# Optimization experiments

Measured on AMD Instinct MI355X. Metric: run time of the kernel, lower is better.

## Reference

```python
import jax, jax.numpy as jnp
import numpy as np

B, V, F, H = 8, 5023, 9976, 512  # batch, n_verts, n_faces, image size (K=1 face per pixel)


def _vertex_normals(verts, faces):
    # verts [V,3], faces [F,3] int. Faithful to DECA util.vertex_normals:
    # cross products scatter-added per face corner, then F.normalize(eps=1e-6).
    v0 = verts[faces[:, 0]]
    v1 = verts[faces[:, 1]]
    v2 = verts[faces[:, 2]]
    n = jnp.zeros_like(verts)
    n = n.at[faces[:, 1]].add(jnp.cross(v2 - v1, v0 - v1))
    n = n.at[faces[:, 2]].add(jnp.cross(v0 - v2, v1 - v2))
    n = n.at[faces[:, 0]].add(jnp.cross(v1 - v0, v2 - v0))
    norm = jnp.maximum(jnp.linalg.norm(n, axis=-1, keepdims=True), 1e-6)
    return n / norm


def _face_vertices(attr, faces):
    # attr [B,V,3] -> [B,F,3,3] gather of per-face corner attributes
    return jax.vmap(lambda a: a[faces])(attr)


def _rasterize_attributes(pix_to_face, bary, attributes):
    # attributes [B,F,3,D]; pix_to_face [N,H,W,K] packed face ids (-1 = miss);
    # bary [N,H,W,K,3]. Mirrors Pytorch3dRasterizer.forward post-raster math.
    Bn, Fn, _, D = attributes.shape
    attrs = attributes.reshape(Bn * Fn, 3, D)
    miss = pix_to_face < 0                              # [N,H,W,K]
    p2f = jnp.where(miss, 0, pix_to_face)
    pixel_face_vals = attrs[p2f]                        # [N,H,W,K,3,D] gather
    pixel_vals = jnp.sum(bary[..., None] * pixel_face_vals, axis=-2)  # [N,H,W,K,D]
    pixel_vals = jnp.where(miss[..., None], 0.0, pixel_vals)
    pixel_vals = jnp.moveaxis(pixel_vals[:, :, :, 0], -1, 1)          # [N,D,H,W]
    vismask = (pix_to_face[..., 0] > -1).astype(pixel_vals.dtype)[:, None]
    return jnp.concatenate([pixel_vals, vismask], axis=1)             # [N,D+1,H,W]


def setup_inputs() -> dict:
    keys = jax.random.split(jax.random.key(0), 8)
    vertices = jax.random.normal(keys[0], (B, V, 3), jnp.float32)
    transformed_vertices = jax.random.normal(keys[1], (B, V, 3), jnp.float32)
    albedos = jax.random.uniform(keys[2], (B, 3, 256, 256), jnp.float32)
    face_uvcoords = jax.random.uniform(keys[3], (F, 3, 3), jnp.float32) * 2.0 - 1.0
    bary = jax.random.uniform(keys[4], (B, H, H, 1, 3), jnp.float32) + 1e-3
    bary_coords = bary / bary.sum(-1, keepdims=True)
    faces = jax.random.randint(keys[5], (F, 3), 0, V, jnp.int32)
    p2f = jax.random.randint(keys[6], (B, H, H, 1), 0, B * F, jnp.int32)
    miss = jax.random.uniform(keys[7], (B, H, H, 1)) < 0.3
    pix_to_face = jnp.where(miss, jnp.int32(-1), p2f)
    return {"vertices": vertices, "transformed_vertices": transformed_vertices,
            "albedos": albedos, "face_uvcoords": face_uvcoords,
            "bary_coords": bary_coords, "faces": faces, "pix_to_face": pix_to_face}


def reference(vertices, transformed_vertices, albedos, face_uvcoords, bary_coords, faces, pix_to_face):
    # albedos is unused in this forward path (shading branch disabled in source).
    del albedos
    batch = vertices.shape[0]
    tv = transformed_vertices.at[:, :, 2].add(10.0)
    face_verts = _face_vertices(vertices, faces)                         # [B,F,3,3]
    normals = jax.vmap(_vertex_normals, in_axes=(0, None))(vertices, faces)
    face_normals = _face_vertices(normals, faces)                        # [B,F,3,3]
    t_normals = jax.vmap(_vertex_normals, in_axes=(0, None))(tv, faces)
    t_face_normals = _face_vertices(t_normals, faces)                    # [B,F,3,3]
    norm_uv = face_uvcoords * 0.5 + 0.5                                  # [F,3,3]
    attributes = jnp.concatenate([
        jnp.broadcast_to(norm_uv[None], (batch,) + norm_uv.shape),
        jax.lax.stop_gradient(t_face_normals),
        jax.lax.stop_gradient(face_verts),
        face_normals,
    ], axis=-1)                                                          # [B,F,3,12]
    rendering = _rasterize_attributes(pix_to_face, bary_coords, attributes)  # [B,13,H,W]
    uvcoords_images = rendering[:, :3]
    grid = jnp.transpose(uvcoords_images, (0, 2, 3, 1))[..., :2]
    t_normal_map = jax.lax.stop_gradient(rendering[:, 3:6])
    pos_mask = (t_normal_map[:, 2:] < -0.05).astype(rendering.dtype)
    normal_images = rendering[:, 9:12]
    return (uvcoords_images, pos_mask, grid, normals, normal_images, t_normals)
```

## Files before the change

### kernel.cpp

```cpp
#include <hip/hip_runtime.h>
#include <hip/hip_fp16.h>

#define BB_ 8
#define VV_ 5023
#define FF_ 9976
#define HH_ 512

static constexpr long long OUT_UV   = 0;
static constexpr long long OUT_POS  = OUT_UV   + (long long)BB_*3*HH_*HH_;
static constexpr long long OUT_GRID = OUT_POS  + (long long)BB_*HH_*HH_;
static constexpr long long OUT_N    = OUT_GRID + (long long)BB_*HH_*HH_*2;
static constexpr long long OUT_NIMG = OUT_N    + (long long)BB_*VV_*3;
static constexpr long long OUT_TN   = OUT_NIMG + (long long)BB_*3*HH_*HH_;

__device__ inline float pack_h2(float a, float b) {
    union { float f; __half2 h; } u;
    u.h = __halves2half2(__float2half_rn(a), __float2half_rn(b));
    return u.f;
}
__device__ inline float2 unpack_h2(float w) {
    union { float f; __half2 h; } u; u.f = w;
    return __half22float2(u.h);
}

__global__ __launch_bounds__(256) void facenorm_k(const float* __restrict__ verts,
                                                  const float* __restrict__ tverts,
                                                  const int*   __restrict__ faces,
                                                  float* __restrict__ fnorm,
                                                  int*   __restrict__ counts) {
    int t = blockIdx.x * blockDim.x + threadIdx.x;
    if (t >= BB_ * 2 * FF_) return;
    int bm = t / FF_;
    int f  = t - bm * FF_;
    int m  = bm & 1;
    int b  = bm >> 1;

    const float* vb = (m ? tverts : verts) + (long long)b * VV_ * 3;
    const float zoff = m ? 10.0f : 0.0f;

    int i0 = faces[f*3+0], i1 = faces[f*3+1], i2 = faces[f*3+2];
    float v0x = vb[i0*3+0], v0y = vb[i0*3+1], v0z = vb[i0*3+2] + zoff;
    float v1x = vb[i1*3+0], v1y = vb[i1*3+1], v1z = vb[i1*3+2] + zoff;
    float v2x = vb[i2*3+0], v2y = vb[i2*3+1], v2z = vb[i2*3+2] + zoff;
    float ax = v1x - v0x, ay = v1y - v0y, az = v1z - v0z;
    float bx = v2x - v0x, by = v2y - v0y, bz = v2z - v0z;
    fnorm[(long long)t*3+0] = ay * bz - az * by;
    fnorm[(long long)t*3+1] = az * bx - ax * bz;
    fnorm[(long long)t*3+2] = ax * by - ay * bx;

    if (bm == 0) {
        atomicAdd(&counts[i0], 1);
        atomicAdd(&counts[i1], 1);
        atomicAdd(&counts[i2], 1);
    }
}

__global__ __launch_bounds__(256) void scan_k(const int* __restrict__ counts,
                                              int* __restrict__ offsets,
                                              int* __restrict__ cursor) {
    __shared__ int sums[256];
    const int SEG = (VV_ + 255) / 256;
    int tid = threadIdx.x;

    int local[SEG];
    int s = 0;
    #pragma unroll
    for (int j = 0; j < SEG; ++j) {
        int v = tid * SEG + j;
        int c = (v < VV_) ? counts[v] : 0;
        local[j] = s;
        s += c;
    }
    sums[tid] = s;
    __syncthreads();
    for (int st = 1; st < 256; st <<= 1) {
        int add = (tid >= st) ? sums[tid - st] : 0;
        __syncthreads();
        sums[tid] += add;
        __syncthreads();
    }
    int base = (tid == 0) ? 0 : sums[tid - 1];
    #pragma unroll
    for (int j = 0; j < SEG; ++j) {
        int v = tid * SEG + j;
        if (v < VV_) {
            int o = base + local[j];
            offsets[v] = o;
            cursor[v]  = o;
        }
    }
    if (tid == 0) offsets[VV_] = FF_ * 3;
}

__global__ __launch_bounds__(256) void fill_k(const int* __restrict__ faces,
                                              int* __restrict__ cursor,
                                              int* __restrict__ list) {
    int i = blockIdx.x * blockDim.x + threadIdx.x;
    if (i >= FF_ * 3) return;
    int v = faces[i];
    int slot = atomicAdd(&cursor[v], 1);
    list[slot] = i / 3;
}

__global__ __launch_bounds__(256) void gather_k(const int* __restrict__ offsets,
                                                const int* __restrict__ list,
                                                const float* __restrict__ fnorm,
                                                float* __restrict__ outN,
                                                float* __restrict__ outTN) {
    int t = blockIdx.x * blockDim.x + threadIdx.x;
    if (t >= BB_ * 2 * VV_) return;
    int bm = t / VV_;
    int v  = t - bm * VV_;
    int o0 = offsets[v], o1 = offsets[v + 1];
    const float* fb = fnorm + (long long)bm * FF_ * 3;
    float x = 0.f, y = 0.f, z = 0.f;
    for (int j = o0; j < o1; ++j) {
        int f = list[j];
        x += fb[f*3+0];
        y += fb[f*3+1];
        z += fb[f*3+2];
    }
    float inv = 1.0f / fmaxf(sqrtf(x*x + y*y + z*z), 1e-6f);
    float* o = ((bm & 1) ? outTN : outN) + ((long long)(bm >> 1) * VV_ + v) * 3;
    o[0] = x * inv; o[1] = y * inv; o[2] = z * inv;
}

__global__ void build_recs(const int*   __restrict__ faces,
                           const float* __restrict__ uvc,
                           const float* __restrict__ outN,
                           const float* __restrict__ outTN,
                           float4* __restrict__ uvrec,
                           float4* __restrict__ nrec) {
    int t = blockIdx.x * blockDim.x + threadIdx.x;
    if (t >= BB_ * FF_) return;
    int b = t / FF_;
    int f = t - b * FF_;
    int ia = faces[f*3+0], ib = faces[f*3+1], ic = faces[f*3+2];

    const float* nb = outN  + (long long)b * VV_ * 3;
    const float* tb = outTN + (long long)b * VV_ * 3;
    float nax = nb[ia*3+0], nay = nb[ia*3+1], naz = nb[ia*3+2];
    float nbx = nb[ib*3+0], nby = nb[ib*3+1], nbz = nb[ib*3+2];
    float ncx = nb[ic*3+0], ncy = nb[ic*3+1], ncz = nb[ic*3+2];
    float ta = tb[ia*3+2], tbv = tb[ib*3+2], tc = tb[ic*3+2];

    nrec[(long long)t*2+0] = make_float4(ta, tbv, tc, pack_h2(ncz, 0.f));
    nrec[(long long)t*2+1] = make_float4(pack_h2(nax, nay), pack_h2(naz, nbx),
                                         pack_h2(nby, nbz), pack_h2(ncx, ncy));

    if (b == 0) {
        const float* u = uvc + (long long)f * 9;
        float r0 = u[0]*0.5f+0.5f, r1 = u[1]*0.5f+0.5f, r2 = u[2]*0.5f+0.5f;
        float r3 = u[3]*0.5f+0.5f, r4 = u[4]*0.5f+0.5f, r5 = u[5]*0.5f+0.5f;
        float r6 = u[6]*0.5f+0.5f, r7 = u[7]*0.5f+0.5f, r8 = u[8]*0.5f+0.5f;
        uvrec[(long long)f*2+0] = make_float4(pack_h2(r0,r1), pack_h2(r2,r3),
                                              pack_h2(r4,r5), pack_h2(r6,r7));
        uvrec[(long long)f*2+1] = make_float4(pack_h2(r8,0.f), 0.f, 0.f, 0.f);
    }
}

__device__ inline void shade(int pf, float w0, float w1, float w2,
                             const float4* __restrict__ uvrec,
                             const float4* __restrict__ nrec,
                             float& uv0, float& uv1, float& uv2,
                             float& n0, float& n1, float& n2, float& pm) {
    int pfs = pf < 0 ? 0 : pf;
    int bb = pfs / FF_;
    int ff = pfs - bb * FF_;

    float4 U0 = uvrec[(long long)ff*2+0];
    float  U8 = ((const float*)uvrec)[(long long)ff*8+4];
    float4 A  = nrec[(long long)pfs*2+0];
    float4 Bq = nrec[(long long)pfs*2+1];

    float2 u01 = unpack_h2(U0.x), u23 = unpack_h2(U0.y);
    float2 u45 = unpack_h2(U0.z), u67 = unpack_h2(U0.w);
    float2 u8p = unpack_h2(U8);
    float2 m01 = unpack_h2(Bq.x), m23 = unpack_h2(Bq.y);
    float2 m45 = unpack_h2(Bq.z), m67 = unpack_h2(Bq.w);
    float2 m8p = unpack_h2(A.w);

    uv0 = w0*u01.x + w1*u23.y + w2*u67.x;
    uv1 = w0*u01.y + w1*u45.x + w2*u67.y;
    uv2 = w0*u23.x + w1*u45.y + w2*u8p.x;
    n0  = w0*m01.x + w1*m23.y + w2*m67.x;
    n1  = w0*m01.y + w1*m45.x + w2*m67.y;
    n2  = w0*m23.x + w1*m45.y + w2*m8p.x;
    float tnz = w0*A.x + w1*A.y + w2*A.z;
    pm = (tnz < -0.05f) ? 1.0f : 0.0f;

    if (pf < 0) { uv0 = uv1 = uv2 = n0 = n1 = n2 = pm = 0.0f; }
}

__global__ __launch_bounds__(256) void raster4(const int4*   __restrict__ p2f4,
                                               const float4* __restrict__ bary4,
                                               const float4* __restrict__ uvrec,
                                               const float4* __restrict__ nrec,
                                               float* __restrict__ out) {
    int t = blockIdx.x * blockDim.x + threadIdx.x;
    const int NQ = BB_ * HH_ * HH_ / 4;
    if (t >= NQ) return;
    int pix0 = t << 2;
    int b    = pix0 >> 18;
    int yx0  = pix0 & (HH_*HH_ - 1);

    int4   pf = p2f4[t];
    float4 B0 = bary4[(long long)t*3+0];
    float4 B1 = bary4[(long long)t*3+1];
    float4 B2 = bary4[(long long)t*3+2];

    float uv0a, uv1a, uv2a, n0a, n1a, n2a, pma;
    float uv0b, uv1b, uv2b, n0b, n1b, n2b, pmb;
    float uv0c, uv1c, uv2c, n0c, n1c, n2c, pmc;
    float uv0d, uv1d, uv2d, n0d, n1d, n2d, pmd;

    shade(pf.x, B0.x, B0.y, B0.z, uvrec, nrec, uv0a, uv1a, uv2a, n0a, n1a, n2a, pma);
    shade(pf.y, B0.w, B1.x, B1.y, uvrec, nrec, uv0b, uv1b, uv2b, n0b, n1b, n2b, pmb);
    shade(pf.z, B1.z, B1.w, B2.x, uvrec, nrec, uv0c, uv1c, uv2c, n0c, n1c, n2c, pmc);
    shade(pf.w, B2.y, B2.z, B2.w, uvrec, nrec, uv0d, uv1d, uv2d, n0d, n1d, n2d, pmd);

    const long long HW = (long long)HH_ * HH_;
    *(float4*)(out + OUT_UV  + ((long long)(b*3+0))*HW + yx0) = make_float4(uv0a, uv0b, uv0c, uv0d);
    *(float4*)(out + OUT_UV  + ((long long)(b*3+1))*HW + yx0) = make_float4(uv1a, uv1b, uv1c, uv1d);
    *(float4*)(out + OUT_UV  + ((long long)(b*3+2))*HW + yx0) = make_float4(uv2a, uv2b, uv2c, uv2d);
    *(float4*)(out + OUT_POS + (long long)b*HW + yx0)         = make_float4(pma, pmb, pmc, pmd);
    float* gbase = out + OUT_GRID + ((long long)b*HW + yx0)*2;
    *(float4*)(gbase + 0) = make_float4(uv0a, uv1a, uv0b, uv1b);
    *(float4*)(gbase + 4) = make_float4(uv0c, uv1c, uv0d, uv1d);
    *(float4*)(out + OUT_NIMG + ((long long)(b*3+0))*HW + yx0) = make_float4(n0a, n0b, n0c, n0d);
    *(float4*)(out + OUT_NIMG + ((long long)(b*3+1))*HW + yx0) = make_float4(n1a, n1b, n1c, n1d);
    *(float4*)(out + OUT_NIMG + ((long long)(b*3+2))*HW + yx0) = make_float4(n2a, n2b, n2c, n2d);
}

extern "C" void kernel_launch(void* const* d_in, const int* in_sizes, int n_in,
                              void* d_out, int out_size, void* d_ws, size_t ws_size,
                              hipStream_t stream) {
    const float* vertices  = (const float*)d_in[0];
    const float* tvertices = (const float*)d_in[1];
    const float* face_uvc  = (const float*)d_in[3];
    const float* bary      = (const float*)d_in[4];
    const int*   faces     = (const int*)d_in[5];
    const int*   p2f       = (const int*)d_in[6];

    float* out = (float*)d_out;

    float4* uvrec   = (float4*)d_ws;
    float4* nrec    = uvrec + (size_t)FF_*2;
    float*  fnorm   = (float*)(nrec + (size_t)BB_*FF_*2);
    int*    counts  = (int*)(fnorm + (size_t)BB_*2*FF_*3);
    int*    offsets = counts + VV_;
    int*    cursor  = offsets + VV_ + 1;
    int*    list    = cursor + VV_;

    hipMemsetAsync(counts, 0, (size_t)VV_ * sizeof(int), stream);

    {
        int n = BB_ * 2 * FF_;
        facenorm_k<<<(n + 255) / 256, 256, 0, stream>>>(vertices, tvertices, faces, fnorm, counts);
    }
    scan_k<<<1, 256, 0, stream>>>(counts, offsets, cursor);
    {
        int n = FF_ * 3;
        fill_k<<<(n + 255) / 256, 256, 0, stream>>>(faces, cursor, list);
    }
    {
        int n = BB_ * 2 * VV_;
        gather_k<<<(n + 255) / 256, 256, 0, stream>>>(offsets, list, fnorm, out + OUT_N, out + OUT_TN);
    }
    {
        int n = BB_ * FF_;
        build_recs<<<(n + 255) / 256, 256, 0, stream>>>(faces, face_uvc, out + OUT_N, out + OUT_TN, uvrec, nrec);
    }
    {
        int nq = BB_ * HH_ * HH_ / 4;
        raster4<<<(nq + 255) / 256, 256, 0, stream>>>((const int4*)p2f, (const float4*)bary,
                                                      uvrec, nrec, out);
    }
}
```

Before: 75.20 us.

## Fuse mesh topology build into one block and recompute face normals in gather

Replaces the memset, count, scan and fill kernels with one single-block kernel that builds the vertex-to-face adjacency in shared memory. The separate face-normal kernel and its scratch buffer are removed; each vertex now recomputes the cross products of its incident faces while gathering. Per-face UV and normal data are packed into one 64-byte record per batch-face, so each pixel does three float4 loads from one record, and miss pixels skip the loads. This removes launches and intermediate traffic at the cost of redundant cross-product work, a serial single-block topology pass, and a larger per-batch record table.

```diff
diff --git a/kernel.cpp b/kernel.cpp
--- a/kernel.cpp
+++ b/kernel.cpp
@@ -23,115 +23,99 @@
     return __half22float2(u.h);
 }
 
-__global__ __launch_bounds__(256) void facenorm_k(const float* __restrict__ verts,
-                                                  const float* __restrict__ tverts,
-                                                  const int*   __restrict__ faces,
-                                                  float* __restrict__ fnorm,
-                                                  int*   __restrict__ counts) {
-    int t = blockIdx.x * blockDim.x + threadIdx.x;
-    if (t >= BB_ * 2 * FF_) return;
-    int bm = t / FF_;
-    int f  = t - bm * FF_;
-    int m  = bm & 1;
-    int b  = bm >> 1;
-
-    const float* vb = (m ? tverts : verts) + (long long)b * VV_ * 3;
-    const float zoff = m ? 10.0f : 0.0f;
-
-    int i0 = faces[f*3+0], i1 = faces[f*3+1], i2 = faces[f*3+2];
-    float v0x = vb[i0*3+0], v0y = vb[i0*3+1], v0z = vb[i0*3+2] + zoff;
-    float v1x = vb[i1*3+0], v1y = vb[i1*3+1], v1z = vb[i1*3+2] + zoff;
-    float v2x = vb[i2*3+0], v2y = vb[i2*3+1], v2z = vb[i2*3+2] + zoff;
-    float ax = v1x - v0x, ay = v1y - v0y, az = v1z - v0z;
-    float bx = v2x - v0x, by = v2y - v0y, bz = v2z - v0z;
-    fnorm[(long long)t*3+0] = ay * bz - az * by;
-    fnorm[(long long)t*3+1] = az * bx - ax * bz;
-    fnorm[(long long)t*3+2] = ax * by - ay * bx;
-
-    if (bm == 0) {
-        atomicAdd(&counts[i0], 1);
-        atomicAdd(&counts[i1], 1);
-        atomicAdd(&counts[i2], 1);
-    }
-}
-
-__global__ __launch_bounds__(256) void scan_k(const int* __restrict__ counts,
-                                              int* __restrict__ offsets,
-                                              int* __restrict__ cursor) {
-    __shared__ int sums[256];
-    const int SEG = (VV_ + 255) / 256;
+__global__ __launch_bounds__(1024) void topo_k(const int* __restrict__ faces,
+                                               int* __restrict__ offsets,
+                                               int* __restrict__ list) {
+    __shared__ int cnt[VV_];
+    __shared__ int sums[1024];
     int tid = threadIdx.x;
 
+    for (int v = tid; v < VV_; v += 1024) cnt[v] = 0;
+    __syncthreads();
+    for (int i = tid; i < FF_ * 3; i += 1024) atomicAdd(&cnt[faces[i]], 1);
+    __syncthreads();
+
+    const int SEG = (VV_ + 1023) / 1024;
     int local[SEG];
     int s = 0;
     #pragma unroll
     for (int j = 0; j < SEG; ++j) {
         int v = tid * SEG + j;
-        int c = (v < VV_) ? counts[v] : 0;
+        int c = (v < VV_) ? cnt[v] : 0;
         local[j] = s;
         s += c;
     }
     sums[tid] = s;
     __syncthreads();
-    for (int st = 1; st < 256; st <<= 1) {
+    for (int st = 1; st < 1024; st <<= 1) {
         int add = (tid >= st) ? sums[tid - st] : 0;
         __syncthreads();
         sums[tid] += add;
         __syncthreads();
     }
     int base = (tid == 0) ? 0 : sums[tid - 1];
+    __syncthreads();
     #pragma unroll
     for (int j = 0; j < SEG; ++j) {
         int v = tid * SEG + j;
         if (v < VV_) {
             int o = base + local[j];
             offsets[v] = o;
-            cursor[v]  = o;
+            cnt[v] = o;
         }
     }
     if (tid == 0) offsets[VV_] = FF_ * 3;
-}
-
-__global__ __launch_bounds__(256) void fill_k(const int* __restrict__ faces,
-                                              int* __restrict__ cursor,
-                                              int* __restrict__ list) {
-    int i = blockIdx.x * blockDim.x + threadIdx.x;
-    if (i >= FF_ * 3) return;
-    int v = faces[i];
-    int slot = atomicAdd(&cursor[v], 1);
-    list[slot] = i / 3;
-}
-
-__global__ __launch_bounds__(256) void gather_k(const int* __restrict__ offsets,
-                                                const int* __restrict__ list,
-                                                const float* __restrict__ fnorm,
+    __syncthreads();
+
+    for (int i = tid; i < FF_ * 3; i += 1024) {
+        int v = faces[i];
+        int slot = atomicAdd(&cnt[v], 1);
+        list[slot] = i / 3;
+    }
+}
+
+__global__ __launch_bounds__(64) void vgather_k(const float* __restrict__ verts,
+                                                const float* __restrict__ tverts,
+                                                const int*   __restrict__ faces,
+                                                const int*   __restrict__ offsets,
+                                                const int*   __restrict__ list,
                                                 float* __restrict__ outN,
                                                 float* __restrict__ outTN) {
-    int t = blockIdx.x * blockDim.x + threadIdx.x;
+    int t = blockIdx.x * 64 + threadIdx.x;
     if (t >= BB_ * 2 * VV_) return;
     int bm = t / VV_;
     int v  = t - bm * VV_;
+    int m  = bm & 1;
+    int b  = bm >> 1;
+
+    const float* vb = (m ? tverts : verts) + (long long)b * VV_ * 3;
+    const float zoff = m ? 10.0f : 0.0f;
+
     int o0 = offsets[v], o1 = offsets[v + 1];
-    const float* fb = fnorm + (long long)bm * FF_ * 3;
     float x = 0.f, y = 0.f, z = 0.f;
     for (int j = o0; j < o1; ++j) {
         int f = list[j];
-        x += fb[f*3+0];
-        y += fb[f*3+1];
-        z += fb[f*3+2];
+        int i0 = faces[f*3+0], i1 = faces[f*3+1], i2 = faces[f*3+2];
+        float v0x = vb[i0*3+0], v0y = vb[i0*3+1], v0z = vb[i0*3+2] + zoff;
+        float v1x = vb[i1*3+0], v1y = vb[i1*3+1], v1z = vb[i1*3+2] + zoff;
+        float v2x = vb[i2*3+0], v2y = vb[i2*3+1], v2z = vb[i2*3+2] + zoff;
+        float ax = v1x - v0x, ay = v1y - v0y, az = v1z - v0z;
+        float bx = v2x - v0x, by = v2y - v0y, bz = v2z - v0z;
+        x += ay * bz - az * by;
+        y += az * bx - ax * bz;
+        z += ax * by - ay * bx;
     }
     float inv = 1.0f / fmaxf(sqrtf(x*x + y*y + z*z), 1e-6f);
-    float* o = ((bm & 1) ? outTN : outN) + ((long long)(bm >> 1) * VV_ + v) * 3;
+    float* o = (m ? outTN : outN) + ((long long)b * VV_ + v) * 3;
     o[0] = x * inv; o[1] = y * inv; o[2] = z * inv;
 }
 
-__global__ void build_recs(const int*   __restrict__ faces,
-                           const float* __restrict__ uvc,
-                           const float* __restrict__ outN,
-                           const float* __restrict__ outTN,
-                           float4* __restrict__ uvrec,
-                           float4* __restrict__ nrec) {
-    int t = blockIdx.x * blockDim.x + threadIdx.x;
+__global__ __launch_bounds__(128) void build_rec64(const int*   __restrict__ faces,
+                                                   const float* __restrict__ uvc,
+                                                   const float* __restrict__ outN,
+                                                   const float* __restrict__ outTN,
+                                                   float4* __restrict__ rec) {
+    int t = blockIdx.x * 128 + threadIdx.x;
     if (t >= BB_ * FF_) return;
     int b = t / FF_;
     int f = t - b * FF_;
@@ -144,58 +128,45 @@
     float ncx = nb[ic*3+0], ncy = nb[ic*3+1], ncz = nb[ic*3+2];
     float ta = tb[ia*3+2], tbv = tb[ib*3+2], tc = tb[ic*3+2];
 
-    nrec[(long long)t*2+0] = make_float4(ta, tbv, tc, pack_h2(ncz, 0.f));
-    nrec[(long long)t*2+1] = make_float4(pack_h2(nax, nay), pack_h2(naz, nbx),
-                                         pack_h2(nby, nbz), pack_h2(ncx, ncy));
-
-    if (b == 0) {
-        const float* u = uvc + (long long)f * 9;
-        float r0 = u[0]*0.5f+0.5f, r1 = u[1]*0.5f+0.5f, r2 = u[2]*0.5f+0.5f;
-        float r3 = u[3]*0.5f+0.5f, r4 = u[4]*0.5f+0.5f, r5 = u[5]*0.5f+0.5f;
-        float r6 = u[6]*0.5f+0.5f, r7 = u[7]*0.5f+0.5f, r8 = u[8]*0.5f+0.5f;
-        uvrec[(long long)f*2+0] = make_float4(pack_h2(r0,r1), pack_h2(r2,r3),
-                                              pack_h2(r4,r5), pack_h2(r6,r7));
-        uvrec[(long long)f*2+1] = make_float4(pack_h2(r8,0.f), 0.f, 0.f, 0.f);
-    }
+    const float* u = uvc + (long long)f * 9;
+    float r0 = u[0]*0.5f+0.5f, r1 = u[1]*0.5f+0.5f, r2 = u[2]*0.5f+0.5f;
+    float r3 = u[3]*0.5f+0.5f, r4 = u[4]*0.5f+0.5f, r5 = u[5]*0.5f+0.5f;
+    float r6 = u[6]*0.5f+0.5f, r7 = u[7]*0.5f+0.5f, r8 = u[8]*0.5f+0.5f;
+
+    float4* o = rec + (long long)t * 4;
+    o[0] = make_float4(ta, tbv, tc, pack_h2(r8, ncz));
+    o[1] = make_float4(pack_h2(r0,r1), pack_h2(r2,r3), pack_h2(r4,r5), pack_h2(r6,r7));
+    o[2] = make_float4(pack_h2(nax,nay), pack_h2(naz,nbx), pack_h2(nby,nbz), pack_h2(ncx,ncy));
 }
 
 __device__ inline void shade(int pf, float w0, float w1, float w2,
-                             const float4* __restrict__ uvrec,
-                             const float4* __restrict__ nrec,
+                             const float4* __restrict__ rec,
                              float& uv0, float& uv1, float& uv2,
                              float& n0, float& n1, float& n2, float& pm) {
-    int pfs = pf < 0 ? 0 : pf;
-    int bb = pfs / FF_;
-    int ff = pfs - bb * FF_;
-
-    float4 U0 = uvrec[(long long)ff*2+0];
-    float  U8 = ((const float*)uvrec)[(long long)ff*8+4];
-    float4 A  = nrec[(long long)pfs*2+0];
-    float4 Bq = nrec[(long long)pfs*2+1];
-
-    float2 u01 = unpack_h2(U0.x), u23 = unpack_h2(U0.y);
-    float2 u45 = unpack_h2(U0.z), u67 = unpack_h2(U0.w);
-    float2 u8p = unpack_h2(U8);
-    float2 m01 = unpack_h2(Bq.x), m23 = unpack_h2(Bq.y);
-    float2 m45 = unpack_h2(Bq.z), m67 = unpack_h2(Bq.w);
-    float2 m8p = unpack_h2(A.w);
+    uv0 = uv1 = uv2 = n0 = n1 = n2 = pm = 0.0f;
+    if (pf < 0) return;
+    const float4* R = rec + (long long)pf * 4;
+    float4 q0 = R[0], q1 = R[1], q2 = R[2];
+
+    float2 u8c = unpack_h2(q0.w);
+    float2 u01 = unpack_h2(q1.x), u23 = unpack_h2(q1.y);
+    float2 u45 = unpack_h2(q1.z), u67 = unpack_h2(q1.w);
+    float2 m01 = unpack_h2(q2.x), m23 = unpack_h2(q2.y);
+    float2 m45 = unpack_h2(q2.z), m67 = unpack_h2(q2.w);
 
     uv0 = w0*u01.x + w1*u23.y + w2*u67.x;
     uv1 = w0*u01.y + w1*u45.x + w2*u67.y;
-    uv2 = w0*u23.x + w1*u45.y + w2*u8p.x;
+    uv2 = w0*u23.x + w1*u45.y + w2*u8c.x;
     n0  = w0*m01.x + w1*m23.y + w2*m67.x;
     n1  = w0*m01.y + w1*m45.x + w2*m67.y;
-    n2  = w0*m23.x + w1*m45.y + w2*m8p.x;
-    float tnz = w0*A.x + w1*A.y + w2*A.z;
+    n2  = w0*m23.x + w1*m45.y + w2*u8c.y;
+    float tnz = w0*q0.x + w1*q0.y + w2*q0.z;
     pm = (tnz < -0.05f) ? 1.0f : 0.0f;
-
-    if (pf < 0) { uv0 = uv1 = uv2 = n0 = n1 = n2 = pm = 0.0f; }
-}
-
-__global__ __launch_bounds__(256) void raster4(const int4*   __restrict__ p2f4,
+}
+
+__global__ __launch_bounds__(256) void raster5(const int4*   __restrict__ p2f4,
                                                const float4* __restrict__ bary4,
-                                               const float4* __restrict__ uvrec,
-                                               const float4* __restrict__ nrec,
+                                               const float4* __restrict__ rec,
                                                float* __restrict__ out) {
     int t = blockIdx.x * blockDim.x + threadIdx.x;
     const int NQ = BB_ * HH_ * HH_ / 4;
@@ -214,10 +185,10 @@
     float uv0c, uv1c, uv2c, n0c, n1c, n2c, pmc;
     float uv0d, uv1d, uv2d, n0d, n1d, n2d, pmd;
 
-    shade(pf.x, B0.x, B0.y, B0.z, uvrec, nrec, uv0a, uv1a, uv2a, n0a, n1a, n2a, pma);
-    shade(pf.y, B0.w, B1.x, B1.y, uvrec, nrec, uv0b, uv1b, uv2b, n0b, n1b, n2b, pmb);
-    shade(pf.z, B1.z, B1.w, B2.x, uvrec, nrec, uv0c, uv1c, uv2c, n0c, n1c, n2c, pmc);
-    shade(pf.w, B2.y, B2.z, B2.w, uvrec, nrec, uv0d, uv1d, uv2d, n0d, n1d, n2d, pmd);
+    shade(pf.x, B0.x, B0.y, B0.z, rec, uv0a, uv1a, uv2a, n0a, n1a, n2a, pma);
+    shade(pf.y, B0.w, B1.x, B1.y, rec, uv0b, uv1b, uv2b, n0b, n1b, n2b, pmb);
+    shade(pf.z, B1.z, B1.w, B2.x, rec, uv0c, uv1c, uv2c, n0c, n1c, n2c, pmc);
+    shade(pf.w, B2.y, B2.z, B2.w, rec, uv0d, uv1d, uv2d, n0d, n1d, n2d, pmd);
 
     const long long HW = (long long)HH_ * HH_;
     *(float4*)(out + OUT_UV  + ((long long)(b*3+0))*HW + yx0) = make_float4(uv0a, uv0b, uv0c, uv0d);
@@ -244,36 +215,24 @@
 
     float* out = (float*)d_out;
 
-    float4* uvrec   = (float4*)d_ws;
-    float4* nrec    = uvrec + (size_t)FF_*2;
-    float*  fnorm   = (float*)(nrec + (size_t)BB_*FF_*2);
-    int*    counts  = (int*)(fnorm + (size_t)BB_*2*FF_*3);
-    int*    offsets = counts + VV_;
-    int*    cursor  = offsets + VV_ + 1;
-    int*    list    = cursor + VV_;
-
-    hipMemsetAsync(counts, 0, (size_t)VV_ * sizeof(int), stream);
-
-    {
-        int n = BB_ * 2 * FF_;
-        facenorm_k<<<(n + 255) / 256, 256, 0, stream>>>(vertices, tvertices, faces, fnorm, counts);
-    }
-    scan_k<<<1, 256, 0, stream>>>(counts, offsets, cursor);
-    {
-        int n = FF_ * 3;
-        fill_k<<<(n + 255) / 256, 256, 0, stream>>>(faces, cursor, list);
-    }
+    float4* rec     = (float4*)d_ws;
+    int*    offsets = (int*)(rec + (size_t)BB_ * FF_ * 4);
+    int*    list    = offsets + VV_ + 1;
+
+    topo_k<<<1, 1024, 0, stream>>>(faces, offsets, list);
     {
         int n = BB_ * 2 * VV_;
-        gather_k<<<(n + 255) / 256, 256, 0, stream>>>(offsets, list, fnorm, out + OUT_N, out + OUT_TN);
+        vgather_k<<<(n + 63) / 64, 64, 0, stream>>>(vertices, tvertices, faces,
+                                                    offsets, list, out + OUT_N, out + OUT_TN);
     }
     {
         int n = BB_ * FF_;
-        build_recs<<<(n + 255) / 256, 256, 0, stream>>>(faces, face_uvc, out + OUT_N, out + OUT_TN, uvrec, nrec);
+        build_rec64<<<(n + 127) / 128, 128, 0, stream>>>(faces, face_uvc,
+                                                         out + OUT_N, out + OUT_TN, rec);
     }
     {
         int nq = BB_ * HH_ * HH_ / 4;
-        raster4<<<(nq + 255) / 256, 256, 0, stream>>>((const int4*)p2f, (const float4*)bary,
-                                                      uvrec, nrec, out);
-    }
-}
+        raster5<<<(nq + 255) / 256, 256, 0, stream>>>((const int4*)p2f, (const float4*)bary,
+                                                      rec, out);
+    }
+}
```

Result: slower. 87.94 us (+16.9%).
